# Performance work log

Measured on AMD Instinct MI355X. Metric: run time of the kernel, lower is better.

Reference implementation:

```python
import jax, jax.numpy as jnp
import numpy as np
from jax import lax

EPS = 1e-10
DELU_P = 10.0

def delu(x):
    # delu_feature_map: param*relu(x) + (exp(param*min(x,0)) - 1) + 1
    x1 = jax.nn.relu(x)
    x2 = jnp.exp(DELU_P * (x - x1)) - 1.0
    return DELU_P * x1 + x2 + 1.0

def conv1x1(x, w, b):
    # x: (B,C,H,W), w: (O,C), b: (O,)
    return jnp.einsum('bchw,oc->bohw', x, w) + b[None, :, None, None]

def conv3x3(x, w, b):
    # w: (O,I,3,3), SAME padding, stride 1
    y = lax.conv_general_dilated(x, w, window_strides=(1, 1), padding='SAME',
                                 dimension_numbers=('NCHW', 'OIHW', 'NCHW'))
    return y + b[None, :, None, None]

def setup_inputs() -> dict:
    key = jax.random.key(0)
    ks = jax.random.split(key, 12)
    B, C, H, W = 4, 256, 128, 128
    s = 0.02
    return {
        'x':   jax.random.normal(ks[0], (B, C, H, W), dtype=jnp.float32),
        'wq':  jax.random.normal(ks[1], (C, C), dtype=jnp.float32) * s,
        'bq':  jax.random.normal(ks[2], (C,), dtype=jnp.float32) * s,
        'wk':  jax.random.normal(ks[3], (C, C), dtype=jnp.float32) * s,
        'bk':  jax.random.normal(ks[4], (C,), dtype=jnp.float32) * s,
        'wv':  jax.random.normal(ks[5], (C, C), dtype=jnp.float32) * s,
        'bv':  jax.random.normal(ks[6], (C,), dtype=jnp.float32) * s,
        'wd1': jax.random.normal(ks[7], (C, C), dtype=jnp.float32) * s,
        'bd1': jax.random.normal(ks[8], (C,), dtype=jnp.float32) * s,
        'wd3': jax.random.normal(ks[9], (C, C, 3, 3), dtype=jnp.float32) * s,
        'bd3': jax.random.normal(ks[10], (C,), dtype=jnp.float32) * s,
        'gamma': jax.random.normal(ks[11], (1,), dtype=jnp.float32) * 0.1,
    }

def reference(x, wq, bq, wk, bk, wv, bv, wd1, bd1, wd3, bd3, gamma):
    B, C, H, W = x.shape
    N = H * W
    # q/k/v projections flattened to (B, C, N)
    q = conv1x1(x, wq, bq).reshape(B, C, N)
    k = conv1x1(x, wk, bk).reshape(B, C, N)
    v = conv1x1(x, wv, bv).reshape(B, C, N)
    # feature maps (torch permutes q to (B,N,C), applies map, permutes back -> elementwise, no-op layout)
    q = delu(q)
    k = delu(k)
    # energy: (B, C, C), contracting over spatial N (q indexed 'bmn')
    energy = jnp.einsum('bmn,bcn->bmc', q, k)
    KV = k * v  # (B, C, N) elementwise
    norm = 1.0 / (jnp.einsum('bmc,bcn->bn', energy, k) + EPS)  # (B, N)
    # attention: sum over m of energy, times KV, times norm -> (B, C, N)
    attention = jnp.einsum('bmc,bcn,bn->bcn', energy, KV, norm)
    out = attention.reshape(B, C, H, W)
    out = out + conv1x1(x, wd1, bd1) + conv3x3(x, wd3, bd3)
    return x + gamma[0] * out
```

## Files before the change

kernel.cpp:

```cpp
#include <hip/hip_runtime.h>

#define BB 4
#define CC 256
#define HH 128
#define WW 128
#define NN (HH*WW)
#define EPSF 1e-10f

#define XR 130
#define XPB ((size_t)XR*XR*CC)

typedef __bf16 bf16x8 __attribute__((ext_vector_type(8)));
typedef float  f32x4  __attribute__((ext_vector_type(4)));

__device__ __forceinline__ float delu_f(float v) {
    return v > 0.0f ? fmaf(10.0f, v, 1.0f) : __expf(10.0f * v);
}

__device__ __forceinline__ void gl_lds16(const __bf16* g, __bf16* l) {
    __builtin_amdgcn_global_load_lds(
        (const __attribute__((address_space(1))) void*)g,
        (__attribute__((address_space(3))) void*)l, 16, 0, 0);
}

__global__ __launch_bounds__(256) void k_prep(const float* __restrict__ wq,
    const float* __restrict__ wk, const float* __restrict__ wv,
    const float* __restrict__ wd1, const float* __restrict__ wd3,
    __bf16* __restrict__ wqb, __bf16* __restrict__ wkb, __bf16* __restrict__ wvb,
    __bf16* __restrict__ wcv)
{
    int idx = blockIdx.x * 256 + threadIdx.x;
    if (idx >= CC*CC) return;
    const int oc = idx >> 8, ic = idx & 255;
    const int kb = ic >> 5, ocf = oc >> 4;
    const int lane = ((ic >> 3) & 3)*16 + (oc & 15);
    const int e = ic & 7;
    const size_t off = ((size_t)(kb*16 + ocf)*64 + lane)*8 + e;
    wqb[off] = (__bf16)wq[idx];
    wkb[off] = (__bf16)wk[idx];
    wvb[off] = (__bf16)wv[idx];
    float w9[9];
    #pragma unroll
    for (int k=0;k<9;k++) w9[k] = wd3[(size_t)idx*9 + k];
    w9[4] += wd1[idx];
    #pragma unroll
    for (int t=0;t<9;t++) wcv[(size_t)t*CC*CC + off] = (__bf16)w9[t];
}

__global__ __launch_bounds__(256) void k_xpad(const float* __restrict__ x,
                                              __bf16* __restrict__ xpad)
{
    const int xrow = blockIdx.x;
    const int b    = blockIdx.y;
    const int tid  = threadIdx.x;
    const int hr   = xrow - 1;
    const float* xb = x + (size_t)b*CC*NN;
    __bf16* xpb = xpad + (size_t)b*XPB + (size_t)xrow*XR*CC;
    const bool rowok = (hr >= 0 && hr < HH);
    for (int t = tid; t < XR*32; t += 256) {
        int xcol = t % XR, icg = t / XR;
        int wc = xcol - 1;
        bf16x8 v8 = {};
        if (rowok && wc >= 0 && wc < WW) {
            const float* p = xb + (size_t)(icg*8)*NN + hr*WW + wc;
            #pragma unroll
            for (int j=0;j<8;j++) v8[j] = (__bf16)p[(size_t)j*NN];
        }
        *(bf16x8*)&xpb[(size_t)xcol*CC + icg*8] = v8;
    }
}

__device__ __forceinline__ void stage_tile_async(const __bf16* __restrict__ xrb,
                                                 __bf16* __restrict__ xs,
                                                 int wid, int lane)
{
    #pragma unroll
    for (int j = 0; j < 8; ++j) {
        const int kq = wid + 4*j;
        gl_lds16(xrb + (size_t)lane*CC + kq*8, &xs[(size_t)kq*64*8]);
    }
}

__device__ __forceinline__ void mfma_gemm_l(const __bf16* __restrict__ wb,
                                            const __bf16* __restrict__ xs,
                                            int ocf0, int lane, int l15, int lq,
                                            f32x4 acc[4][4])
{
    #pragma unroll
    for (int kb=0; kb<8; kb++) {
        bf16x8 af[4], bfr[4];
        #pragma unroll
        for (int f=0; f<4; f++)
            af[f] = *(const bf16x8*)&wb[(size_t)((kb*16 + ocf0 + f)*64 + lane)*8];
        #pragma unroll
        for (int nf=0; nf<4; nf++)
            bfr[nf] = *(const bf16x8*)&xs[(size_t)((kb*4 + lq)*64 + nf*16 + l15)*8];
        #pragma unroll
        for (int f=0; f<4; f++)
            #pragma unroll
            for (int nf=0; nf<4; nf++)
                acc[f][nf] = __builtin_amdgcn_mfma_f32_16x16x32_bf16(af[f], bfr[nf], acc[f][nf], 0, 0, 0);
    }
}

__global__ __launch_bounds__(256) void k_qk_mfma(const __bf16* __restrict__ xpad,
    const __bf16* __restrict__ wqb, const float* __restrict__ bq,
    const __bf16* __restrict__ wkb, const float* __restrict__ bk,
    __bf16* __restrict__ kp, float* __restrict__ Qs)
{
    __shared__ __bf16 xs[32*64*8];
    __shared__ float Qpart[4][64];
    const int n0 = blockIdx.x * 64;
    const int b  = blockIdx.y;
    const int tid = threadIdx.x;
    const int wid = tid >> 6, lane = tid & 63;
    const int l15 = lane & 15, lq = lane >> 4;
    const int oc_base = wid*64;
    const int h = n0 >> 7, w0 = n0 & 127;
    const __bf16* xrb = xpad + (size_t)b*XPB + ((size_t)(h+1)*XR + w0 + 1)*CC;

    stage_tile_async(xrb, xs, wid, lane);
    __syncthreads();

    f32x4 acc[4][4] = {};
    mfma_gemm_l(wqb, xs, wid*4, lane, l15, lq, acc);
    #pragma unroll
    for (int nf=0; nf<4; nf++) {
        float s = 0.0f;
        #pragma unroll
        for (int f=0; f<4; f++)
            #pragma unroll
            for (int r=0; r<4; r++)
                s += delu_f(acc[f][nf][r] + bq[oc_base + f*16 + lq*4 + r]);
        s += __shfl_xor(s, 16);
        s += __shfl_xor(s, 32);
        if (lq == 0) Qpart[wid][nf*16 + l15] = s;
    }
    __syncthreads();
    if (tid < 64)
        Qs[(size_t)b*NN + n0 + tid] = Qpart[0][tid] + Qpart[1][tid] + Qpart[2][tid] + Qpart[3][tid];

    #pragma unroll
    for (int f=0; f<4; f++)
        #pragma unroll
        for (int nf=0; nf<4; nf++)
            acc[f][nf] = (f32x4){0.f,0.f,0.f,0.f};
    mfma_gemm_l(wkb, xs, wid*4, lane, l15, lq, acc);
    #pragma unroll
    for (int f=0; f<4; f++) {
        #pragma unroll
        for (int r=0; r<4; r++) {
            const int oc = oc_base + f*16 + lq*4 + r;
            const float bias = bk[oc];
            __bf16* kr = kp + ((size_t)b*CC + oc)*NN + n0;
            #pragma unroll
            for (int nf=0; nf<4; nf++)
                kr[nf*16 + l15] = (__bf16)delu_f(acc[f][nf][r] + bias);
        }
    }
}

__global__ __launch_bounds__(256) void k_esum(const __bf16* __restrict__ kp,
    const float* __restrict__ Qs, float* __restrict__ Es)
{
    const int c = blockIdx.x & (CC-1), b = blockIdx.x >> 8;
    const int tid = threadIdx.x;
    const bf16x8* kr = (const bf16x8*)(kp + ((size_t)b*CC + c)*NN);
    const float4* qr = (const float4*)(Qs + (size_t)b*NN);
    float s = 0.0f;
    for (int i = tid; i < NN/8; i += 256) {
        bf16x8 kk = kr[i];
        float4 q0 = qr[2*i], q1 = qr[2*i+1];
        s += (float)kk[0]*q0.x + (float)kk[1]*q0.y + (float)kk[2]*q0.z + (float)kk[3]*q0.w
           + (float)kk[4]*q1.x + (float)kk[5]*q1.y + (float)kk[6]*q1.z + (float)kk[7]*q1.w;
    }
    #pragma unroll
    for (int m=1; m<64; m<<=1) s += __shfl_xor(s, m, 64);
    __shared__ float red[4];
    if ((tid & 63) == 0) red[tid >> 6] = s;
    __syncthreads();
    if (tid == 0) Es[b*CC + c] = red[0] + red[1] + red[2] + red[3];
}

__global__ __launch_bounds__(256) void k_vattn_mfma(const float* __restrict__ x,
    const __bf16* __restrict__ xpad,
    const __bf16* __restrict__ wvb, const float* __restrict__ bv,
    const __bf16* __restrict__ kp, const float* __restrict__ Es,
    const float* __restrict__ gamma, float* __restrict__ out)
{
    __shared__ __bf16 xs[32*64*8];
    __shared__ float Dpart[4][64];
    __shared__ float rn_sh[64];
    const int n0 = blockIdx.x * 64;
    const int b  = blockIdx.y;
    const int tid = threadIdx.x;
    const int wid = tid >> 6, lane = tid & 63;
    const int l15 = lane & 15, lq = lane >> 4;
    const int oc_base = wid*64;
    const int h = n0 >> 7, w0 = n0 & 127;
    const __bf16* xrb = xpad + (size_t)b*XPB + ((size_t)(h+1)*XR + w0 + 1)*CC;

    stage_tile_async(xrb, xs, wid, lane);
    __syncthreads();

    f32x4 acc[4][4] = {};
    mfma_gemm_l(wvb, xs, wid*4, lane, l15, lq, acc);

    float dpart[4] = {0.f,0.f,0.f,0.f};
    #pragma unroll
    for (int f=0; f<4; f++) {
        #pragma unroll
        for (int r=0; r<4; r++) {
            const int oc = oc_base + f*16 + lq*4 + r;
            const float e = Es[b*CC + oc];
            const __bf16* kr = kp + ((size_t)b*CC + oc)*NN + n0;
            #pragma unroll
            for (int nf=0; nf<4; nf++)
                dpart[nf] = fmaf(e, (float)kr[nf*16 + l15], dpart[nf]);
        }
    }
    #pragma unroll
    for (int nf=0; nf<4; nf++) {
        dpart[nf] += __shfl_xor(dpart[nf], 16);
        dpart[nf] += __shfl_xor(dpart[nf], 32);
        if (lq == 0) Dpart[wid][nf*16 + l15] = dpart[nf];
    }
    __syncthreads();
    if (tid < 64)
        rn_sh[tid] = 1.0f / (Dpart[0][tid] + Dpart[1][tid] + Dpart[2][tid] + Dpart[3][tid] + EPSF);
    __syncthreads();

    const float g = gamma[0];
    float rv[4];
    #pragma unroll
    for (int nf=0; nf<4; nf++) rv[nf] = rn_sh[nf*16 + l15];
    #pragma unroll
    for (int f=0; f<4; f++) {
        #pragma unroll
        for (int r=0; r<4; r++) {
            const int oc = oc_base + f*16 + lq*4 + r;
            const float eg = Es[b*CC + oc] * g;
            const float bias = bv[oc];
            const __bf16* kr = kp + ((size_t)b*CC + oc)*NN + n0;
            const float* xr  = x  + ((size_t)b*CC + oc)*NN + n0;
            float* orow = out + ((size_t)b*CC + oc)*NN + n0;
            #pragma unroll
            for (int nf=0; nf<4; nf++) {
                const int w = nf*16 + l15;
                orow[w] = fmaf(eg*(float)kr[w]*rv[nf], acc[f][nf][r] + bias, xr[w]);
            }
        }
    }
}

__global__ __launch_bounds__(256,2) void k_conv_mfma(const __bf16* __restrict__ xpad,
    const __bf16* __restrict__ wcv, const float* __restrict__ bd1,
    const float* __restrict__ bd3, const float* __restrict__ gamma,
    float* __restrict__ out)
{
    __shared__ __bf16 xs[2][12*132*8];
    const int orig = blockIdx.x;
    const int wg   = (orig & 7)*128 + (orig >> 3);
    const int b    = wg >> 8;
    const int h    = (wg & 255) >> 1;
    const int ocb  = wg & 1;
    const int tid = threadIdx.x;
    const int wid = tid >> 6, lane = tid & 63;
    const int wm = wid >> 1, wn = wid & 1;
    const int l15 = lane & 15, lq = lane >> 4;
    const int oc_base  = ocb*128 + wm*64;
    const int ocf0     = ocb*8 + wm*4;
    const int col_base = wn*64;
    const __bf16* xpb = xpad + (size_t)b*XPB;

    f32x4 acc[4][4] = {};

    #define STAGE_CV(bufsel, icb) do {                                          \
        const int ic0_ = (icb)*32;                                              \
        _Pragma("unroll")                                                       \
        for (int j = 0; j < 9; ++j) {                                           \
            const int w_ = wid + 4*j;                                           \
            const int pair_ = w_ / 3, chunk_ = w_ % 3;                          \
            const int r_ = pair_ >> 2, icq_ = pair_ & 3;                        \
            const int col0_ = chunk_ * 64;                                      \
            if (col0_ + lane < XR)                                              \
                gl_lds16(xpb + ((size_t)(h + r_)*XR + col0_ + lane)*CC + ic0_ + icq_*8, \
                         &xs[bufsel][(size_t)(pair_*132 + col0_)*8]);           \
        }                                                                       \
    } while (0)

    STAGE_CV(0, 0);
    __syncthreads();

    #pragma unroll 1
    for (int icb = 0; icb < 8; ++icb) {
        const __bf16* xb = xs[icb & 1];
        bf16x8 af2[2][4], br2[2][4];
        #pragma unroll
        for (int f=0; f<4; f++)
            af2[0][f] = *(const bf16x8*)&wcv[(size_t)((icb*16 + ocf0 + f)*64 + lane)*8];
        if (icb < 7) STAGE_CV((icb+1)&1, icb+1);
        #pragma unroll
        for (int nf=0; nf<4; nf++)
            br2[0][nf] = *(const bf16x8*)&xb[(size_t)(lq*132 + col_base + nf*16 + l15)*8];
        #pragma unroll
        for (int t=0; t<9; ++t) {
            const int cur = t & 1, nxt = cur ^ 1;
            if (t < 8) {
                const int tn = t + 1, kyn = tn/3, kxn = tn%3;
                #pragma unroll
                for (int f=0; f<4; f++)
                    af2[nxt][f] = *(const bf16x8*)&wcv[(size_t)(((tn*8 + icb)*16 + ocf0 + f)*64 + lane)*8];
                #pragma unroll
                for (int nf=0; nf<4; nf++)
                    br2[nxt][nf] = *(const bf16x8*)&xb[(size_t)((kyn*4 + lq)*132 + col_base + nf*16 + l15 + kxn)*8];
            }
            __builtin_amdgcn_s_setprio(1);
            #pragma unroll
            for (int f=0; f<4; f++)
                #pragma unroll
                for (int nf=0; nf<4; nf++)
                    acc[f][nf] = __builtin_amdgcn_mfma_f32_16x16x32_bf16(af2[cur][f], br2[cur][nf], acc[f][nf], 0, 0, 0);
            __builtin_amdgcn_s_setprio(0);
        }
        __syncthreads();
    }
    #undef STAGE_CV

    const float g = gamma[0];
    #pragma unroll
    for (int f=0; f<4; f++) {
        #pragma unroll
        for (int r=0; r<4; r++) {
            const int oc = oc_base + f*16 + lq*4 + r;
            const float bias = bd1[oc] + bd3[oc];
            float* orow = out + ((size_t)b*CC + oc)*NN + (size_t)h*WW;
            #pragma unroll
            for (int nf=0; nf<4; nf++) {
                const int w = col_base + nf*16 + l15;
                orow[w] += g*(acc[f][nf][r] + bias);
            }
        }
    }
}

extern "C" void kernel_launch(void* const* d_in, const int* in_sizes, int n_in,
                              void* d_out, int out_size, void* d_ws, size_t ws_size,
                              hipStream_t stream)
{
    const float* x     = (const float*)d_in[0];
    const float* wq    = (const float*)d_in[1];
    const float* bq    = (const float*)d_in[2];
    const float* wk    = (const float*)d_in[3];
    const float* bk    = (const float*)d_in[4];
    const float* wv    = (const float*)d_in[5];
    const float* bv    = (const float*)d_in[6];
    const float* wd1   = (const float*)d_in[7];
    const float* bd1   = (const float*)d_in[8];
    const float* wd3   = (const float*)d_in[9];
    const float* bd3   = (const float*)d_in[10];
    const float* gamma = (const float*)d_in[11];
    float* out = (float*)d_out;

    __bf16* kp   = (__bf16*)d_ws;
    float*  Qs   = (float*)(kp + (size_t)BB*CC*NN);
    float*  Es   = Qs + (size_t)BB*NN;
    __bf16* wcv  = (__bf16*)(Es + (size_t)BB*CC);
    __bf16* wqb  = wcv + (size_t)9*CC*CC;
    __bf16* wkb  = wqb + (size_t)CC*CC;
    __bf16* wvb  = wkb + (size_t)CC*CC;
    __bf16* xpad = wvb + (size_t)CC*CC;

    k_prep      <<<dim3(CC*CC/256), 256, 0, stream>>>(wq, wk, wv, wd1, wd3, wqb, wkb, wvb, wcv);
    k_xpad      <<<dim3(XR, BB), 256, 0, stream>>>(x, xpad);
    k_qk_mfma   <<<dim3(NN/64, BB), 256, 0, stream>>>(xpad, wqb, bq, wkb, bk, kp, Qs);
    k_esum      <<<dim3(BB*CC), 256, 0, stream>>>(kp, Qs, Es);
    k_vattn_mfma<<<dim3(NN/64, BB), 256, 0, stream>>>(x, xpad, wvb, bv, kp, Es, gamma, out);
    k_conv_mfma <<<dim3(2*HH*BB), 256, 0, stream>>>(xpad, wcv, bd1, bd3, gamma, out);
}
```

Before: 197.4 us.

## Fuse V projection and attention epilogue into conv kernel, fold energy into QK

The energy reduction is moved into the QK kernel: each block writes per-channel partial sums of Qsum*K, and a small reduction kernel adds them. A separate normalization kernel computes 1/(E·K) per pixel. The V projection is folded into the 3x3 conv kernel by reusing the centre-tap input fragment, so the attention output, conv output and residual are written in one pass. This removes the standalone V/attention kernel, a full read-modify-write of the output, and the reread of K in the energy kernel. In exchange it adds extra MFMA work and a second accumulator set inside the conv loop, which raises register pressure.

```diff
diff --git a/kernel.cpp b/kernel.cpp
--- a/kernel.cpp
+++ b/kernel.cpp
@@ -11,6 +11,7 @@
 #define XPB ((size_t)XR*XR*CC)
 
 typedef __bf16 bf16x8 __attribute__((ext_vector_type(8)));
+typedef __bf16 bf16x4 __attribute__((ext_vector_type(4)));
 typedef float  f32x4  __attribute__((ext_vector_type(4)));
 
 __device__ __forceinline__ float delu_f(float v) {
@@ -106,11 +107,13 @@
 __global__ __launch_bounds__(256) void k_qk_mfma(const __bf16* __restrict__ xpad,
     const __bf16* __restrict__ wqb, const float* __restrict__ bq,
     const __bf16* __restrict__ wkb, const float* __restrict__ bk,
-    __bf16* __restrict__ kp, float* __restrict__ Qs)
+    __bf16* __restrict__ kp, float* __restrict__ Epart)
 {
     __shared__ __bf16 xs[32*64*8];
     __shared__ float Qpart[4][64];
+    __shared__ float qs_sh[64];
     const int n0 = blockIdx.x * 64;
+    const int blk = blockIdx.x;
     const int b  = blockIdx.y;
     const int tid = threadIdx.x;
     const int wid = tid >> 6, lane = tid & 63;
@@ -138,7 +141,8 @@
     }
     __syncthreads();
     if (tid < 64)
-        Qs[(size_t)b*NN + n0 + tid] = Qpart[0][tid] + Qpart[1][tid] + Qpart[2][tid] + Qpart[3][tid];
+        qs_sh[tid] = Qpart[0][tid] + Qpart[1][tid] + Qpart[2][tid] + Qpart[3][tid];
+    __syncthreads();
 
     #pragma unroll
     for (int f=0; f<4; f++)
@@ -146,6 +150,10 @@
         for (int nf=0; nf<4; nf++)
             acc[f][nf] = (f32x4){0.f,0.f,0.f,0.f};
     mfma_gemm_l(wkb, xs, wid*4, lane, l15, lq, acc);
+
+    float qsv[4];
+    #pragma unroll
+    for (int nf=0; nf<4; nf++) qsv[nf] = qs_sh[nf*16 + l15];
     #pragma unroll
     for (int f=0; f<4; f++) {
         #pragma unroll
@@ -153,109 +161,62 @@
             const int oc = oc_base + f*16 + lq*4 + r;
             const float bias = bk[oc];
             __bf16* kr = kp + ((size_t)b*CC + oc)*NN + n0;
-            #pragma unroll
-            for (int nf=0; nf<4; nf++)
-                kr[nf*16 + l15] = (__bf16)delu_f(acc[f][nf][r] + bias);
+            float p = 0.0f;
+            #pragma unroll
+            for (int nf=0; nf<4; nf++) {
+                float kv = delu_f(acc[f][nf][r] + bias);
+                kr[nf*16 + l15] = (__bf16)kv;
+                p = fmaf(qsv[nf], kv, p);
+            }
+            p += __shfl_xor(p, 1); p += __shfl_xor(p, 2);
+            p += __shfl_xor(p, 4); p += __shfl_xor(p, 8);
+            if (l15 == 0)
+                Epart[((size_t)b*256 + blk)*CC + oc] = p;
         }
     }
 }
 
-__global__ __launch_bounds__(256) void k_esum(const __bf16* __restrict__ kp,
-    const float* __restrict__ Qs, float* __restrict__ Es)
-{
-    const int c = blockIdx.x & (CC-1), b = blockIdx.x >> 8;
+__global__ __launch_bounds__(256) void k_ered(const float* __restrict__ Epart,
+                                              float* __restrict__ Es)
+{
+    const int b = blockIdx.x, c = threadIdx.x;
+    float s = 0.0f;
+    const float* p = Epart + (size_t)b*256*CC + c;
+    #pragma unroll 8
+    for (int blk=0; blk<256; blk++) s += p[(size_t)blk*CC];
+    Es[b*CC + c] = s;
+}
+
+__global__ __launch_bounds__(256) void k_norm(const __bf16* __restrict__ kp,
+    const float* __restrict__ Es, float* __restrict__ rn)
+{
+    const int b = blockIdx.y;
+    const int n = blockIdx.x*1024 + threadIdx.x*4;
     const int tid = threadIdx.x;
-    const bf16x8* kr = (const bf16x8*)(kp + ((size_t)b*CC + c)*NN);
-    const float4* qr = (const float4*)(Qs + (size_t)b*NN);
-    float s = 0.0f;
-    for (int i = tid; i < NN/8; i += 256) {
-        bf16x8 kk = kr[i];
-        float4 q0 = qr[2*i], q1 = qr[2*i+1];
-        s += (float)kk[0]*q0.x + (float)kk[1]*q0.y + (float)kk[2]*q0.z + (float)kk[3]*q0.w
-           + (float)kk[4]*q1.x + (float)kk[5]*q1.y + (float)kk[6]*q1.z + (float)kk[7]*q1.w;
-    }
-    #pragma unroll
-    for (int m=1; m<64; m<<=1) s += __shfl_xor(s, m, 64);
-    __shared__ float red[4];
-    if ((tid & 63) == 0) red[tid >> 6] = s;
-    __syncthreads();
-    if (tid == 0) Es[b*CC + c] = red[0] + red[1] + red[2] + red[3];
-}
-
-__global__ __launch_bounds__(256) void k_vattn_mfma(const float* __restrict__ x,
-    const __bf16* __restrict__ xpad,
-    const __bf16* __restrict__ wvb, const float* __restrict__ bv,
-    const __bf16* __restrict__ kp, const float* __restrict__ Es,
-    const float* __restrict__ gamma, float* __restrict__ out)
-{
-    __shared__ __bf16 xs[32*64*8];
-    __shared__ float Dpart[4][64];
-    __shared__ float rn_sh[64];
-    const int n0 = blockIdx.x * 64;
-    const int b  = blockIdx.y;
-    const int tid = threadIdx.x;
-    const int wid = tid >> 6, lane = tid & 63;
-    const int l15 = lane & 15, lq = lane >> 4;
-    const int oc_base = wid*64;
-    const int h = n0 >> 7, w0 = n0 & 127;
-    const __bf16* xrb = xpad + (size_t)b*XPB + ((size_t)(h+1)*XR + w0 + 1)*CC;
-
-    stage_tile_async(xrb, xs, wid, lane);
-    __syncthreads();
-
-    f32x4 acc[4][4] = {};
-    mfma_gemm_l(wvb, xs, wid*4, lane, l15, lq, acc);
-
-    float dpart[4] = {0.f,0.f,0.f,0.f};
-    #pragma unroll
-    for (int f=0; f<4; f++) {
-        #pragma unroll
-        for (int r=0; r<4; r++) {
-            const int oc = oc_base + f*16 + lq*4 + r;
-            const float e = Es[b*CC + oc];
-            const __bf16* kr = kp + ((size_t)b*CC + oc)*NN + n0;
-            #pragma unroll
-            for (int nf=0; nf<4; nf++)
-                dpart[nf] = fmaf(e, (float)kr[nf*16 + l15], dpart[nf]);
-        }
-    }
-    #pragma unroll
-    for (int nf=0; nf<4; nf++) {
-        dpart[nf] += __shfl_xor(dpart[nf], 16);
-        dpart[nf] += __shfl_xor(dpart[nf], 32);
-        if (lq == 0) Dpart[wid][nf*16 + l15] = dpart[nf];
-    }
-    __syncthreads();
-    if (tid < 64)
-        rn_sh[tid] = 1.0f / (Dpart[0][tid] + Dpart[1][tid] + Dpart[2][tid] + Dpart[3][tid] + EPSF);
-    __syncthreads();
-
-    const float g = gamma[0];
-    float rv[4];
-    #pragma unroll
-    for (int nf=0; nf<4; nf++) rv[nf] = rn_sh[nf*16 + l15];
-    #pragma unroll
-    for (int f=0; f<4; f++) {
-        #pragma unroll
-        for (int r=0; r<4; r++) {
-            const int oc = oc_base + f*16 + lq*4 + r;
-            const float eg = Es[b*CC + oc] * g;
-            const float bias = bv[oc];
-            const __bf16* kr = kp + ((size_t)b*CC + oc)*NN + n0;
-            const float* xr  = x  + ((size_t)b*CC + oc)*NN + n0;
-            float* orow = out + ((size_t)b*CC + oc)*NN + n0;
-            #pragma unroll
-            for (int nf=0; nf<4; nf++) {
-                const int w = nf*16 + l15;
-                orow[w] = fmaf(eg*(float)kr[w]*rv[nf], acc[f][nf][r] + bias, xr[w]);
-            }
-        }
-    }
-}
-
-__global__ __launch_bounds__(256,2) void k_conv_mfma(const __bf16* __restrict__ xpad,
-    const __bf16* __restrict__ wcv, const float* __restrict__ bd1,
-    const float* __restrict__ bd3, const float* __restrict__ gamma,
+    __shared__ float es[CC];
+    es[tid] = Es[b*CC + tid];
+    __syncthreads();
+    float a[4] = {0.f,0.f,0.f,0.f};
+    const __bf16* kb = kp + (size_t)b*CC*NN + n;
+    #pragma unroll 4
+    for (int c=0;c<CC;c++) {
+        bf16x4 kk = *(const bf16x4*)&kb[(size_t)c*NN];
+        const float e = es[c];
+        #pragma unroll
+        for (int j=0;j<4;j++) a[j] = fmaf(e, (float)kk[j], a[j]);
+    }
+    float4 o;
+    o.x = 1.0f/(a[0]+EPSF); o.y = 1.0f/(a[1]+EPSF);
+    o.z = 1.0f/(a[2]+EPSF); o.w = 1.0f/(a[3]+EPSF);
+    *(float4*)&rn[(size_t)b*NN + n] = o;
+}
+
+__global__ __launch_bounds__(256,2) void k_fused(const __bf16* __restrict__ xpad,
+    const __bf16* __restrict__ wcv, const __bf16* __restrict__ wvb,
+    const float* __restrict__ bv, const __bf16* __restrict__ kp,
+    const float* __restrict__ Es, const float* __restrict__ rn,
+    const float* __restrict__ bd1, const float* __restrict__ bd3,
+    const float* __restrict__ gamma, const float* __restrict__ x,
     float* __restrict__ out)
 {
     __shared__ __bf16 xs[2][12*132*8];
@@ -274,6 +235,7 @@
     const __bf16* xpb = xpad + (size_t)b*XPB;
 
     f32x4 acc[4][4] = {};
+    f32x4 accV[4][4] = {};
 
     #define STAGE_CV(bufsel, icb) do {                                          \
         const int ic0_ = (icb)*32;                                              \
@@ -295,10 +257,13 @@
     #pragma unroll 1
     for (int icb = 0; icb < 8; ++icb) {
         const __bf16* xb = xs[icb & 1];
-        bf16x8 af2[2][4], br2[2][4];
+        bf16x8 af2[2][4], br2[2][4], afv[4];
         #pragma unroll
         for (int f=0; f<4; f++)
             af2[0][f] = *(const bf16x8*)&wcv[(size_t)((icb*16 + ocf0 + f)*64 + lane)*8];
+        #pragma unroll
+        for (int f=0; f<4; f++)
+            afv[f] = *(const bf16x8*)&wvb[(size_t)((icb*16 + ocf0 + f)*64 + lane)*8];
         if (icb < 7) STAGE_CV((icb+1)&1, icb+1);
         #pragma unroll
         for (int nf=0; nf<4; nf++)
@@ -321,6 +286,13 @@
                 #pragma unroll
                 for (int nf=0; nf<4; nf++)
                     acc[f][nf] = __builtin_amdgcn_mfma_f32_16x16x32_bf16(af2[cur][f], br2[cur][nf], acc[f][nf], 0, 0, 0);
+            if (t == 4) {
+                #pragma unroll
+                for (int f=0; f<4; f++)
+                    #pragma unroll
+                    for (int nf=0; nf<4; nf++)
+                        accV[f][nf] = __builtin_amdgcn_mfma_f32_16x16x32_bf16(afv[f], br2[cur][nf], accV[f][nf], 0, 0, 0);
+            }
             __builtin_amdgcn_s_setprio(0);
         }
         __syncthreads();
@@ -328,17 +300,26 @@
     #undef STAGE_CV
 
     const float g = gamma[0];
+    float rv[4];
+    #pragma unroll
+    for (int nf=0; nf<4; nf++)
+        rv[nf] = rn[(size_t)b*NN + h*WW + col_base + nf*16 + l15];
     #pragma unroll
     for (int f=0; f<4; f++) {
         #pragma unroll
         for (int r=0; r<4; r++) {
             const int oc = oc_base + f*16 + lq*4 + r;
-            const float bias = bd1[oc] + bd3[oc];
+            const float biasd = bd1[oc] + bd3[oc];
+            const float bv_   = bv[oc];
+            const float es_   = Es[b*CC + oc];
+            const __bf16* kr = kp + ((size_t)b*CC + oc)*NN + (size_t)h*WW;
+            const float*  xr = x  + ((size_t)b*CC + oc)*NN + (size_t)h*WW;
             float* orow = out + ((size_t)b*CC + oc)*NN + (size_t)h*WW;
             #pragma unroll
             for (int nf=0; nf<4; nf++) {
                 const int w = col_base + nf*16 + l15;
-                orow[w] += g*(acc[f][nf][r] + bias);
+                const float attn = es_ * (float)kr[w] * rv[nf] * (accV[f][nf][r] + bv_);
+                orow[w] = fmaf(g, attn + acc[f][nf][r] + biasd, xr[w]);
             }
         }
     }
@@ -362,19 +343,21 @@
     const float* gamma = (const float*)d_in[11];
     float* out = (float*)d_out;
 
-    __bf16* kp   = (__bf16*)d_ws;
-    float*  Qs   = (float*)(kp + (size_t)BB*CC*NN);
-    float*  Es   = Qs + (size_t)BB*NN;
-    __bf16* wcv  = (__bf16*)(Es + (size_t)BB*CC);
-    __bf16* wqb  = wcv + (size_t)9*CC*CC;
-    __bf16* wkb  = wqb + (size_t)CC*CC;
-    __bf16* wvb  = wkb + (size_t)CC*CC;
-    __bf16* xpad = wvb + (size_t)CC*CC;
-
-    k_prep      <<<dim3(CC*CC/256), 256, 0, stream>>>(wq, wk, wv, wd1, wd3, wqb, wkb, wvb, wcv);
-    k_xpad      <<<dim3(XR, BB), 256, 0, stream>>>(x, xpad);
-    k_qk_mfma   <<<dim3(NN/64, BB), 256, 0, stream>>>(xpad, wqb, bq, wkb, bk, kp, Qs);
-    k_esum      <<<dim3(BB*CC), 256, 0, stream>>>(kp, Qs, Es);
-    k_vattn_mfma<<<dim3(NN/64, BB), 256, 0, stream>>>(x, xpad, wvb, bv, kp, Es, gamma, out);
-    k_conv_mfma <<<dim3(2*HH*BB), 256, 0, stream>>>(xpad, wcv, bd1, bd3, gamma, out);
-}
+    __bf16* kp    = (__bf16*)d_ws;
+    float*  Es    = (float*)(kp + (size_t)BB*CC*NN);
+    float*  Epart = Es + (size_t)BB*CC;
+    float*  rn    = Epart + (size_t)BB*256*CC;
+    __bf16* wcv   = (__bf16*)(rn + (size_t)BB*NN);
+    __bf16* wqb   = wcv + (size_t)9*CC*CC;
+    __bf16* wkb   = wqb + (size_t)CC*CC;
+    __bf16* wvb   = wkb + (size_t)CC*CC;
+    __bf16* xpad  = wvb + (size_t)CC*CC;
+
+    k_prep   <<<dim3(CC*CC/256), 256, 0, stream>>>(wq, wk, wv, wd1, wd3, wqb, wkb, wvb, wcv);
+    k_xpad   <<<dim3(XR, BB), 256, 0, stream>>>(x, xpad);
+    k_qk_mfma<<<dim3(NN/64, BB), 256, 0, stream>>>(xpad, wqb, bq, wkb, bk, kp, Epart);
+    k_ered   <<<dim3(BB), 256, 0, stream>>>(Epart, Es);
+    k_norm   <<<dim3(NN/1024, BB), 256, 0, stream>>>(kp, Es, rn);
+    k_fused  <<<dim3(2*HH*BB), 256, 0, stream>>>(xpad, wcv, wvb, bv, kp, Es, rn,
+                                                 bd1, bd3, gamma, x, out);
+}
```

Measured after the change: 279.2 us. 41.5% more time.

## Fuse energy partial sums into qk kernel epilogue, replace esum with small reduction

Applied to the files above, without the earlier changes.

The q·k per-channel reduction is computed in the qk kernel's epilogue while k values are still in registers. Per-block partials are written to a workspace and summed by a small reduction kernel. This removes the separate pass that re-read the whole bf16 k tensor from global memory. In exchange it adds an extra barrier, shuffles and partial writes, and a low-parallelism final reduction kernel.

```diff
diff --git a/kernel.cpp b/kernel.cpp
--- a/kernel.cpp
+++ b/kernel.cpp
@@ -106,11 +106,13 @@
 __global__ __launch_bounds__(256) void k_qk_mfma(const __bf16* __restrict__ xpad,
     const __bf16* __restrict__ wqb, const float* __restrict__ bq,
     const __bf16* __restrict__ wkb, const float* __restrict__ bk,
-    __bf16* __restrict__ kp, float* __restrict__ Qs)
+    __bf16* __restrict__ kp, float* __restrict__ Epart)
 {
     __shared__ __bf16 xs[32*64*8];
     __shared__ float Qpart[4][64];
+    __shared__ float qs_sh[64];
     const int n0 = blockIdx.x * 64;
+    const int blk = blockIdx.x;
     const int b  = blockIdx.y;
     const int tid = threadIdx.x;
     const int wid = tid >> 6, lane = tid & 63;
@@ -138,7 +140,8 @@
     }
     __syncthreads();
     if (tid < 64)
-        Qs[(size_t)b*NN + n0 + tid] = Qpart[0][tid] + Qpart[1][tid] + Qpart[2][tid] + Qpart[3][tid];
+        qs_sh[tid] = Qpart[0][tid] + Qpart[1][tid] + Qpart[2][tid] + Qpart[3][tid];
+    __syncthreads();
 
     #pragma unroll
     for (int f=0; f<4; f++)
@@ -146,6 +149,10 @@
         for (int nf=0; nf<4; nf++)
             acc[f][nf] = (f32x4){0.f,0.f,0.f,0.f};
     mfma_gemm_l(wkb, xs, wid*4, lane, l15, lq, acc);
+
+    float qsv[4];
+    #pragma unroll
+    for (int nf=0; nf<4; nf++) qsv[nf] = qs_sh[nf*16 + l15];
     #pragma unroll
     for (int f=0; f<4; f++) {
         #pragma unroll
@@ -153,33 +160,30 @@
             const int oc = oc_base + f*16 + lq*4 + r;
             const float bias = bk[oc];
             __bf16* kr = kp + ((size_t)b*CC + oc)*NN + n0;
-            #pragma unroll
-            for (int nf=0; nf<4; nf++)
-                kr[nf*16 + l15] = (__bf16)delu_f(acc[f][nf][r] + bias);
-        }
-    }
-}
-
-__global__ __launch_bounds__(256) void k_esum(const __bf16* __restrict__ kp,
-    const float* __restrict__ Qs, float* __restrict__ Es)
-{
-    const int c = blockIdx.x & (CC-1), b = blockIdx.x >> 8;
-    const int tid = threadIdx.x;
-    const bf16x8* kr = (const bf16x8*)(kp + ((size_t)b*CC + c)*NN);
-    const float4* qr = (const float4*)(Qs + (size_t)b*NN);
+            float p = 0.0f;
+            #pragma unroll
+            for (int nf=0; nf<4; nf++) {
+                float kv = delu_f(acc[f][nf][r] + bias);
+                kr[nf*16 + l15] = (__bf16)kv;
+                p = fmaf(qsv[nf], kv, p);
+            }
+            p += __shfl_xor(p, 1); p += __shfl_xor(p, 2);
+            p += __shfl_xor(p, 4); p += __shfl_xor(p, 8);
+            if (l15 == 0)
+                Epart[((size_t)b*256 + blk)*CC + oc] = p;
+        }
+    }
+}
+
+__global__ __launch_bounds__(256) void k_ered(const float* __restrict__ Epart,
+                                              float* __restrict__ Es)
+{
+    const int b = blockIdx.x, c = threadIdx.x;
     float s = 0.0f;
-    for (int i = tid; i < NN/8; i += 256) {
-        bf16x8 kk = kr[i];
-        float4 q0 = qr[2*i], q1 = qr[2*i+1];
-        s += (float)kk[0]*q0.x + (float)kk[1]*q0.y + (float)kk[2]*q0.z + (float)kk[3]*q0.w
-           + (float)kk[4]*q1.x + (float)kk[5]*q1.y + (float)kk[6]*q1.z + (float)kk[7]*q1.w;
-    }
-    #pragma unroll
-    for (int m=1; m<64; m<<=1) s += __shfl_xor(s, m, 64);
-    __shared__ float red[4];
-    if ((tid & 63) == 0) red[tid >> 6] = s;
-    __syncthreads();
-    if (tid == 0) Es[b*CC + c] = red[0] + red[1] + red[2] + red[3];
+    const float* p = Epart + (size_t)b*256*CC + c;
+    #pragma unroll 8
+    for (int blk=0; blk<256; blk++) s += p[(size_t)blk*CC];
+    Es[b*CC + c] = s;
 }
 
 __global__ __launch_bounds__(256) void k_vattn_mfma(const float* __restrict__ x,
@@ -362,19 +366,19 @@
     const float* gamma = (const float*)d_in[11];
     float* out = (float*)d_out;
 
-    __bf16* kp   = (__bf16*)d_ws;
-    float*  Qs   = (float*)(kp + (size_t)BB*CC*NN);
-    float*  Es   = Qs + (size_t)BB*NN;
-    __bf16* wcv  = (__bf16*)(Es + (size_t)BB*CC);
-    __bf16* wqb  = wcv + (size_t)9*CC*CC;
-    __bf16* wkb  = wqb + (size_t)CC*CC;
-    __bf16* wvb  = wkb + (size_t)CC*CC;
-    __bf16* xpad = wvb + (size_t)CC*CC;
+    __bf16* kp    = (__bf16*)d_ws;
+    float*  Es    = (float*)(kp + (size_t)BB*CC*NN);
+    float*  Epart = Es + (size_t)BB*CC;
+    __bf16* wcv   = (__bf16*)(Epart + (size_t)BB*256*CC);
+    __bf16* wqb   = wcv + (size_t)9*CC*CC;
+    __bf16* wkb   = wqb + (size_t)CC*CC;
+    __bf16* wvb   = wkb + (size_t)CC*CC;
+    __bf16* xpad  = wvb + (size_t)CC*CC;
 
     k_prep      <<<dim3(CC*CC/256), 256, 0, stream>>>(wq, wk, wv, wd1, wd3, wqb, wkb, wvb, wcv);
     k_xpad      <<<dim3(XR, BB), 256, 0, stream>>>(x, xpad);
-    k_qk_mfma   <<<dim3(NN/64, BB), 256, 0, stream>>>(xpad, wqb, bq, wkb, bk, kp, Qs);
-    k_esum      <<<dim3(BB*CC), 256, 0, stream>>>(kp, Qs, Es);
+    k_qk_mfma   <<<dim3(NN/64, BB), 256, 0, stream>>>(xpad, wqb, bq, wkb, bk, kp, Epart);
+    k_ered      <<<dim3(BB), 256, 0, stream>>>(Epart, Es);
     k_vattn_mfma<<<dim3(NN/64, BB), 256, 0, stream>>>(x, xpad, wvb, bv, kp, Es, gamma, out);
     k_conv_mfma <<<dim3(2*HH*BB), 256, 0, stream>>>(xpad, wcv, bd1, bd3, gamma, out);
 }
```

Measured after the change: 208.3 us. 5.5% more time.

## Switch 3x3 conv to 32x32x16 MFMA with full-channel workgroups per row

Applied to the files above, without the earlier changes.

The conv kernel moves from 16x16x32 bf16 MFMA to 32x32x16 bf16 MFMA, with weights repacked in the prep kernel into a matching 32-row fragment layout. Each workgroup now covers all 256 output channels for one image row (four waves of 64 channels each), which halves the grid and stages each input row tile into LDS once instead of twice. The B fragments are read from LDS inside the MFMA loop instead of being double-buffered in registers. The intent is fewer LDS reads and less redundant input staging per FLOP. The cost is larger per-wave accumulators, a smaller grid (512 workgroups), and LDS read latency that is no longer prefetched.

```diff
diff --git a/kernel.cpp b/kernel.cpp
--- a/kernel.cpp
+++ b/kernel.cpp
@@ -12,6 +12,7 @@
 
 typedef __bf16 bf16x8 __attribute__((ext_vector_type(8)));
 typedef float  f32x4  __attribute__((ext_vector_type(4)));
+typedef float  f32x16 __attribute__((ext_vector_type(16)));
 
 __device__ __forceinline__ float delu_f(float v) {
     return v > 0.0f ? fmaf(10.0f, v, 1.0f) : __expf(10.0f * v);
@@ -27,7 +28,7 @@
     const float* __restrict__ wk, const float* __restrict__ wv,
     const float* __restrict__ wd1, const float* __restrict__ wd3,
     __bf16* __restrict__ wqb, __bf16* __restrict__ wkb, __bf16* __restrict__ wvb,
-    __bf16* __restrict__ wcv)
+    __bf16* __restrict__ wcv32)
 {
     int idx = blockIdx.x * 256 + threadIdx.x;
     if (idx >= CC*CC) return;
@@ -39,12 +40,16 @@
     wqb[off] = (__bf16)wq[idx];
     wkb[off] = (__bf16)wk[idx];
     wvb[off] = (__bf16)wv[idx];
+    const int ocf32 = oc >> 5;
+    const int gks = ic >> 4, khi = (ic >> 3) & 1;
+    const int lane32 = khi*32 + (oc & 31);
+    const size_t off32 = ((size_t)((gks*8 + ocf32))*64 + lane32)*8 + e;
     float w9[9];
     #pragma unroll
     for (int k=0;k<9;k++) w9[k] = wd3[(size_t)idx*9 + k];
     w9[4] += wd1[idx];
     #pragma unroll
-    for (int t=0;t<9;t++) wcv[(size_t)t*CC*CC + off] = (__bf16)w9[t];
+    for (int t=0;t<9;t++) wcv32[(size_t)t*CC*CC + off32] = (__bf16)w9[t];
 }
 
 __global__ __launch_bounds__(256) void k_xpad(const float* __restrict__ x,
@@ -254,26 +259,22 @@
 }
 
 __global__ __launch_bounds__(256,2) void k_conv_mfma(const __bf16* __restrict__ xpad,
-    const __bf16* __restrict__ wcv, const float* __restrict__ bd1,
+    const __bf16* __restrict__ wcv32, const float* __restrict__ bd1,
     const float* __restrict__ bd3, const float* __restrict__ gamma,
     float* __restrict__ out)
 {
     __shared__ __bf16 xs[2][12*132*8];
     const int orig = blockIdx.x;
-    const int wg   = (orig & 7)*128 + (orig >> 3);
-    const int b    = wg >> 8;
-    const int h    = (wg & 255) >> 1;
-    const int ocb  = wg & 1;
+    const int wg   = (orig & 7)*64 + (orig >> 3);
+    const int b    = wg >> 7;
+    const int h    = wg & 127;
     const int tid = threadIdx.x;
     const int wid = tid >> 6, lane = tid & 63;
-    const int wm = wid >> 1, wn = wid & 1;
-    const int l15 = lane & 15, lq = lane >> 4;
-    const int oc_base  = ocb*128 + wm*64;
-    const int ocf0     = ocb*8 + wm*4;
-    const int col_base = wn*64;
+    const int l31 = lane & 31, lhi = lane >> 5;
+    const int oc_base = wid*64;
     const __bf16* xpb = xpad + (size_t)b*XPB;
 
-    f32x4 acc[4][4] = {};
+    f32x16 acc[2][4] = {};
 
     #define STAGE_CV(bufsel, icb) do {                                          \
         const int ic0_ = (icb)*32;                                              \
@@ -289,56 +290,61 @@
         }                                                                       \
     } while (0)
 
+    #define AF_LOAD(dst, t, icb)                                                \
+        _Pragma("unroll")                                                       \
+        for (int f=0; f<2; f++)                                                 \
+            _Pragma("unroll")                                                   \
+            for (int kk=0; kk<2; kk++)                                          \
+                dst[f*2+kk] = *(const bf16x8*)&wcv32[((size_t)(t)*CC*CC) +      \
+                    ((size_t)((((icb)*2 + kk)*8 + wid*2 + f))*64 + lane)*8];
+
     STAGE_CV(0, 0);
     __syncthreads();
 
     #pragma unroll 1
     for (int icb = 0; icb < 8; ++icb) {
         const __bf16* xb = xs[icb & 1];
-        bf16x8 af2[2][4], br2[2][4];
-        #pragma unroll
-        for (int f=0; f<4; f++)
-            af2[0][f] = *(const bf16x8*)&wcv[(size_t)((icb*16 + ocf0 + f)*64 + lane)*8];
+        bf16x8 af2[2][4];
+        AF_LOAD(af2[0], 0, icb);
         if (icb < 7) STAGE_CV((icb+1)&1, icb+1);
-        #pragma unroll
-        for (int nf=0; nf<4; nf++)
-            br2[0][nf] = *(const bf16x8*)&xb[(size_t)(lq*132 + col_base + nf*16 + l15)*8];
         #pragma unroll
         for (int t=0; t<9; ++t) {
             const int cur = t & 1, nxt = cur ^ 1;
-            if (t < 8) {
-                const int tn = t + 1, kyn = tn/3, kxn = tn%3;
+            const int ky = t/3, kx = t%3;
+            if (t < 8) { AF_LOAD(af2[nxt], t+1, icb); }
+            __builtin_amdgcn_s_setprio(1);
+            #pragma unroll
+            for (int kk=0; kk<2; kk++) {
                 #pragma unroll
-                for (int f=0; f<4; f++)
-                    af2[nxt][f] = *(const bf16x8*)&wcv[(size_t)(((tn*8 + icb)*16 + ocf0 + f)*64 + lane)*8];
-                #pragma unroll
-                for (int nf=0; nf<4; nf++)
-                    br2[nxt][nf] = *(const bf16x8*)&xb[(size_t)((kyn*4 + lq)*132 + col_base + nf*16 + l15 + kxn)*8];
+                for (int nf=0; nf<4; nf++) {
+                    bf16x8 br = *(const bf16x8*)&xs[icb & 1][
+                        (size_t)((ky*4 + kk*2 + lhi)*132 + nf*32 + l31 + kx)*8];
+                    #pragma unroll
+                    for (int f=0; f<2; f++)
+                        acc[f][nf] = __builtin_amdgcn_mfma_f32_32x32x16_bf16(
+                            af2[cur][f*2+kk], br, acc[f][nf], 0, 0, 0);
+                }
             }
-            __builtin_amdgcn_s_setprio(1);
-            #pragma unroll
-            for (int f=0; f<4; f++)
-                #pragma unroll
-                for (int nf=0; nf<4; nf++)
-                    acc[f][nf] = __builtin_amdgcn_mfma_f32_16x16x32_bf16(af2[cur][f], br2[cur][nf], acc[f][nf], 0, 0, 0);
             __builtin_amdgcn_s_setprio(0);
         }
         __syncthreads();
     }
     #undef STAGE_CV
+    #undef AF_LOAD
 
     const float g = gamma[0];
     #pragma unroll
-    for (int f=0; f<4; f++) {
-        #pragma unroll
-        for (int r=0; r<4; r++) {
-            const int oc = oc_base + f*16 + lq*4 + r;
+    for (int f=0; f<2; f++) {
+        #pragma unroll
+        for (int reg=0; reg<16; reg++) {
+            const int row = (reg & 3) + 8*(reg >> 2) + 4*lhi;
+            const int oc = oc_base + f*32 + row;
             const float bias = bd1[oc] + bd3[oc];
             float* orow = out + ((size_t)b*CC + oc)*NN + (size_t)h*WW;
             #pragma unroll
             for (int nf=0; nf<4; nf++) {
-                const int w = col_base + nf*16 + l15;
-                orow[w] += g*(acc[f][nf][r] + bias);
+                const int w = nf*32 + l31;
+                orow[w] += g*(acc[f][nf][reg] + bias);
             }
         }
     }
@@ -362,19 +368,19 @@
     const float* gamma = (const float*)d_in[11];
     float* out = (float*)d_out;
 
-    __bf16* kp   = (__bf16*)d_ws;
-    float*  Qs   = (float*)(kp + (size_t)BB*CC*NN);
-    float*  Es   = Qs + (size_t)BB*NN;
-    __bf16* wcv  = (__bf16*)(Es + (size_t)BB*CC);
-    __bf16* wqb  = wcv + (size_t)9*CC*CC;
-    __bf16* wkb  = wqb + (size_t)CC*CC;
-    __bf16* wvb  = wkb + (size_t)CC*CC;
-    __bf16* xpad = wvb + (size_t)CC*CC;
-
-    k_prep      <<<dim3(CC*CC/256), 256, 0, stream>>>(wq, wk, wv, wd1, wd3, wqb, wkb, wvb, wcv);
+    __bf16* kp    = (__bf16*)d_ws;
+    float*  Qs    = (float*)(kp + (size_t)BB*CC*NN);
+    float*  Es    = Qs + (size_t)BB*NN;
+    __bf16* wcv32 = (__bf16*)(Es + (size_t)BB*CC);
+    __bf16* wqb   = wcv32 + (size_t)9*CC*CC;
+    __bf16* wkb   = wqb + (size_t)CC*CC;
+    __bf16* wvb   = wkb + (size_t)CC*CC;
+    __bf16* xpad  = wvb + (size_t)CC*CC;
+
+    k_prep      <<<dim3(CC*CC/256), 256, 0, stream>>>(wq, wk, wv, wd1, wd3, wqb, wkb, wvb, wcv32);
     k_xpad      <<<dim3(XR, BB), 256, 0, stream>>>(x, xpad);
     k_qk_mfma   <<<dim3(NN/64, BB), 256, 0, stream>>>(xpad, wqb, bq, wkb, bk, kp, Qs);
     k_esum      <<<dim3(BB*CC), 256, 0, stream>>>(kp, Qs, Es);
     k_vattn_mfma<<<dim3(NN/64, BB), 256, 0, stream>>>(x, xpad, wvb, bv, kp, Es, gamma, out);
-    k_conv_mfma <<<dim3(2*HH*BB), 256, 0, stream>>>(xpad, wcv, bd1, bd3, gamma, out);
-}
+    k_conv_mfma <<<dim3(HH*BB), 256, 0, stream>>>(xpad, wcv32, bd1, bd3, gamma, out);
+}
```

After: 190.8 us. 3.3% less time.
